# Optimization experiments

Measured on AMD Instinct MI355X. Metric: run time of the kernel, lower is better.

The kernel has to match this reference:

```python
import jax, jax.numpy as jnp
import numpy as np

FS = 512
SEQ_LEN = 16384
BATCH = 128
TAPS = 513  # common kernel length; per-band kernels zero-padded at the tail
N_BANDS = 20


def _design_kernels():
    """Windowed-sinc (fir1/firwin-style, hamming) bandpass kernels, tensorpac-like."""
    pha = [(f, f + 2.0) for f in np.arange(2.0, 22.0, 2.0)]    # 10 phase bands
    amp = [(f, f + 10.0) for f in np.arange(30.0, 130.0, 10.0)]  # 10 amp bands
    cycles = [3] * 10 + [6] * 10
    bands = pha + amp
    K = np.zeros((N_BANDS, TAPS), np.float32)
    for i, ((lo, hi), c) in enumerate(zip(bands, cycles)):
        order = min(int(c * FS / lo), TAPS - 1)  # fir_order ~ cycle * fs / low_hz
        taps = order + 1
        n = np.arange(taps) - (taps - 1) / 2.0
        f1, f2 = lo / FS, hi / FS
        h = 2.0 * f2 * np.sinc(2.0 * f2 * n) - 2.0 * f1 * np.sinc(2.0 * f1 * n)
        h *= np.hamming(taps)
        K[i, :taps] = h.astype(np.float32)
    return jnp.asarray(K)


def setup_inputs() -> dict:
    key = jax.random.key(0)
    x = jax.random.normal(key, (BATCH, 1, SEQ_LEN), dtype=jnp.float32)
    return {"x": x, "kernels": _design_kernels(), "padlen": TAPS - 1}


def _filtfilt_bands(x2d, kernels, P):
    """scipy.signal.filtfilt(b, 1.0, x, padlen=P) for all bands at once.
    x2d: (B, L); kernels: (nb, T) FIR taps. Odd-extension padding + lfilter_zi
    initial conditions (== constant extension of the first sample by T-1)."""
    B, L = x2d.shape
    nb, T = kernels.shape
    # odd extension: left_j = 2*x[0] - x[P-j], right_j = 2*x[-1] - x[-2-j]
    left = 2.0 * x2d[:, :1] - x2d[:, 1:P + 1][:, ::-1]
    right = 2.0 * x2d[:, -1:] - x2d[:, -P - 1:-1][:, ::-1]
    ext = jnp.concatenate([left, x2d, right], axis=1)  # (B, L + 2P)
    krev = kernels[:, ::-1][:, None, :]  # (nb, 1, T); correlation with b[::-1] == causal conv with b

    def causal_conv(sig, groups):
        # sig: (B, C, Ls); constant left-extension by T-1 (lfilter zi*x0 semantics)
        pad = jnp.repeat(sig[..., :1], T - 1, axis=-1)
        s = jnp.concatenate([pad, sig], axis=-1)
        return jax.lax.conv_general_dilated(
            s, krev, (1,), 'VALID',
            dimension_numbers=('NCW', 'OIW', 'NCW'),
            feature_group_count=groups)

    y = causal_conv(ext[:, None, :], 1)        # forward pass -> (B, nb, L+2P)
    y2 = causal_conv(y[:, :, ::-1], nb)        # backward pass (grouped, per-band)
    return y2[:, :, ::-1][:, :, P:P + L]       # un-reverse and trim padding


def reference(x, kernels, padlen):
    # x: (B, 1, L) -> (B, 1, n_bands, L)
    out = _filtfilt_bands(x[:, 0, :], kernels, padlen)
    return out[:, None, :, :]
```

## Files before the change

kernel.cpp:

```cpp
#include <hip/hip_runtime.h>

#define LSEQ   16384
#define NB     20
#define NBATCH 128
#define TAPS   513
#define CT     (2*TAPS - 1)
#define MAXSTEP 68

#define TT     2048
#define SPANE  3088
#define STRIDE 3096
#define EXTEND 16896
#define GMAX   17407

#define HDR_OFF  0
#define ATAB_OFF 1024

typedef short  v8s  __attribute__((ext_vector_type(8)));
typedef __bf16 v8bf __attribute__((ext_vector_type(8)));
typedef float  v16f __attribute__((ext_vector_type(16)));

__device__ __forceinline__ unsigned short f2bf(float f) {
    union { float f; unsigned u; } v; v.f = f;
    return (unsigned short)((v.u + 0x7fffu + ((v.u >> 16) & 1u)) >> 16);
}

__device__ __forceinline__ v16f vzero() {
    v16f z;
    #pragma unroll
    for (int i = 0; i < 16; ++i) z[i] = 0.f;
    return z;
}

__global__ __launch_bounds__(1024) void prep_kernel(
    const float* __restrict__ Kg, int2* __restrict__ hdr, short* __restrict__ atab)
{
    __shared__ float kk[TAPS];
    __shared__ float Cs[CT];
    __shared__ int smin, smax, sk0, sN;
    const int band = blockIdx.x;
    const int tid  = threadIdx.x;

    for (int i = tid; i < TAPS; i += 1024) kk[i] = Kg[band * TAPS + i];
    if (tid == 0) { smin = CT; smax = 0; }
    __syncthreads();

    int lmin = CT, lmax = 0;
    for (int d = tid; d < CT; d += 1024) {
        int al = d - 512; if (al < 0) al = -al;
        const int n = TAPS - al;
        float s0 = 0.f, s1 = 0.f, s2 = 0.f, s3 = 0.f;
        int i = 0;
        for (; i + 3 < n; i += 4) {
            s0 = fmaf(kk[i],     kk[i + al],     s0);
            s1 = fmaf(kk[i + 1], kk[i + 1 + al], s1);
            s2 = fmaf(kk[i + 2], kk[i + 2 + al], s2);
            s3 = fmaf(kk[i + 3], kk[i + 3 + al], s3);
        }
        for (; i < n; ++i) s0 = fmaf(kk[i], kk[i + al], s0);
        float s = (s0 + s1) + (s2 + s3);
        Cs[d] = s;
        if (s != 0.f) { if (d < lmin) lmin = d; if (d > lmax) lmax = d; }
    }
    atomicMin(&smin, lmin);
    atomicMax(&smax, lmax);
    __syncthreads();

    if (tid == 0) {
        int k0 = smin & ~15;
        int k1 = ((smax + 31) >> 4) << 4;
        int N  = (k1 - k0) / 16 + 1;
        int2 h; h.x = k0; h.y = N;
        hdr[band] = h;
        sk0 = k0; sN = N;
    }
    __syncthreads();

    const int k0 = sk0, N = sN;
    for (int idx = tid; idx < (N + 3) * 64; idx += 1024) {
        int s = idx >> 6, lane = idx & 63;
        int m = lane & 31, kh = lane >> 5;
        int base = k0 + 16 * s + 8 * kh - m;
        v8s r;
        #pragma unroll
        for (int j = 0; j < 8; ++j) {
            int ci = base + j;
            float v = (ci >= 0 && ci < CT) ? Cs[ci] : 0.f;
            r[j] = (short)f2bf(v);
        }
        *(v8s*)(atab + ((size_t)(band * MAXSTEP + s) * 64 + lane) * 8) = r;
    }
}

__global__ __launch_bounds__(256, 3) void filt_main(
    const float* __restrict__ x, const short* __restrict__ atab,
    const int2* __restrict__ hdr, float* __restrict__ out)
{
    __shared__ __align__(16) unsigned short extl[8 * STRIDE];
    const int tid = threadIdx.x;
    const int tile = blockIdx.x, grp = blockIdx.y, bg = blockIdx.z;
    const int T0 = tile * TT;

    const bool edge = (T0 < 512) || (T0 + SPANE > EXTEND);
    for (int b = 0; b < 8; ++b) {
        const float* xb = x + (size_t)(bg * 8 + b) * LSEQ;
        float x0 = 0.f, xN = 0.f;
        if (edge) { x0 = xb[0]; xN = xb[LSEQ - 1]; }
        for (int e4 = tid; e4 < SPANE / 4; e4 += 256) {
            const int e = 4 * e4;
            const int g0 = T0 + e;
            float v0, v1, v2, v3;
            if (g0 >= 512 && g0 + 4 <= EXTEND) {
                float4 xv = *(const float4*)(xb + (g0 - 512));
                v0 = xv.x; v1 = xv.y; v2 = xv.z; v3 = xv.w;
            } else {
                float vv[4];
                #pragma unroll
                for (int t = 0; t < 4; ++t) {
                    int g = g0 + t; if (g > GMAX) g = GMAX;
                    vv[t] = (g < 512)    ? 2.f * x0 - xb[512 - g]
                          : (g < EXTEND) ? xb[g - 512]
                          :                2.f * xN - xb[2 * LSEQ + 512 - 2 - g];
                }
                v0 = vv[0]; v1 = vv[1]; v2 = vv[2]; v3 = vv[3];
            }
            ushort4 q = make_ushort4(f2bf(v0), f2bf(v1), f2bf(v2), f2bf(v3));
            *(ushort4*)&extl[b * STRIDE + e] = q;
        }
    }
    __syncthreads();

    const int lane = tid & 63;
    const int w    = tid >> 6;
    const int n    = lane & 31, kh = lane >> 5;
    const int brow = n & 7,  tb = n >> 3;
    const unsigned short* bpb = extl + brow * STRIDE + 512 * w + 32 * tb + 8 * kh;

    const int g_start[6] = {0, 4, 8, 11, 15, 20};
    const int g_list[20] = {0,19,18,17, 1,16,15,14, 2,3,13, 4,5,6,12, 7,8,9,10,11};

    for (int bi = g_start[grp]; bi < g_start[grp + 1]; ++bi) {
        const int band = g_list[bi];
        const int2 hh = hdr[band];
        const int k0 = hh.x, N = hh.y;
        const unsigned short* bp = bpb + k0;
        const short* ap = atab + (size_t)(band * MAXSTEP) * 512 + lane * 8;

        v16f ac0 = vzero(), ac1 = vzero(), ac2 = vzero(), ac3 = vzero();
        v8bf A0 = __builtin_bit_cast(v8bf, *(const v8s*)ap);
        v8bf A1 = __builtin_bit_cast(v8bf, *(const v8s*)(ap + 512));
        v8bf A2 = __builtin_bit_cast(v8bf, *(const v8s*)(ap + 1024));
        v8bf B0 = *(const v8bf*)(bp);
        v8bf B1 = *(const v8bf*)(bp + 128);
        v8bf B2 = *(const v8bf*)(bp + 256);
        v8bf B3 = *(const v8bf*)(bp + 384);

        for (int s = 0; s < N; ++s) {
            v8bf An  = __builtin_bit_cast(v8bf, *(const v8s*)(ap + (size_t)(s + 3) * 512));
            const unsigned short* bn = bp + 16 * (s + 1);
            v8bf Bn0 = *(const v8bf*)(bn);
            v8bf Bn1 = *(const v8bf*)(bn + 128);
            v8bf Bn2 = *(const v8bf*)(bn + 256);
            v8bf Bn3 = *(const v8bf*)(bn + 384);
            ac0 = __builtin_amdgcn_mfma_f32_32x32x16_bf16(A0, B0, ac0, 0, 0, 0);
            ac1 = __builtin_amdgcn_mfma_f32_32x32x16_bf16(A0, B1, ac1, 0, 0, 0);
            ac2 = __builtin_amdgcn_mfma_f32_32x32x16_bf16(A0, B2, ac2, 0, 0, 0);
            ac3 = __builtin_amdgcn_mfma_f32_32x32x16_bf16(A0, B3, ac3, 0, 0, 0);
            A0 = A1; A1 = A2; A2 = An;
            B0 = Bn0; B1 = Bn1; B2 = Bn2; B3 = Bn3;
        }

        float* ob = out + ((size_t)(bg * 8 + brow) * NB + band) * LSEQ
                        + T0 + 512 * w + 32 * tb + 4 * kh;
        #pragma unroll
        for (int q = 0; q < 4; ++q) {
            *(float4*)(ob +       8 * q) = make_float4(ac0[4*q], ac0[4*q+1], ac0[4*q+2], ac0[4*q+3]);
            *(float4*)(ob + 128 + 8 * q) = make_float4(ac1[4*q], ac1[4*q+1], ac1[4*q+2], ac1[4*q+3]);
            *(float4*)(ob + 256 + 8 * q) = make_float4(ac2[4*q], ac2[4*q+1], ac2[4*q+2], ac2[4*q+3]);
            *(float4*)(ob + 384 + 8 * q) = make_float4(ac3[4*q], ac3[4*q+1], ac3[4*q+2], ac3[4*q+3]);
        }
    }
}

extern "C" void kernel_launch(void* const* d_in, const int* in_sizes, int n_in,
                              void* d_out, int out_size, void* d_ws, size_t ws_size,
                              hipStream_t stream) {
    const float* x  = (const float*)d_in[0];
    const float* Kg = (const float*)d_in[1];
    float* out = (float*)d_out;

    char* wsb = (char*)d_ws;
    int2*  hdr  = (int2*)(wsb + HDR_OFF);
    short* atab = (short*)(wsb + ATAB_OFF);

    prep_kernel<<<dim3(NB), dim3(1024), 0, stream>>>(Kg, hdr, atab);
    filt_main<<<dim3(LSEQ / TT, 5, NBATCH / 8), dim3(256), 0, stream>>>(x, atab, hdr, out);
}
```

Before: 229.0 us.

## Split kernel autocorrelation prep across more blocks and tune MFMA loop

The single 20-block prep kernel, which computed each band's kernel autocorrelation serially per lag, is split into two kernels. The first spreads lags over 9 blocks per band and splits each dot product four ways, reducing through shared memory. The second merges the per-block support bounds and builds the bf16 MFMA A-table. The main filter loop also gets unroll-by-2 and s_setprio around the MFMA group. This adds one extra launch and a workspace round-trip for the autocorrelation to shorten the prep critical path.

```diff
diff --git a/kernel.cpp b/kernel.cpp
--- a/kernel.cpp
+++ b/kernel.cpp
@@ -5,7 +5,7 @@
 #define NBATCH 128
 #define TAPS   513
 #define CT     (2*TAPS - 1)
-#define MAXSTEP 68
+#define MAXSTEP 72
 
 #define TT     2048
 #define SPANE  3088
@@ -14,7 +14,10 @@
 #define GMAX   17407
 
 #define HDR_OFF  0
-#define ATAB_OFF 1024
+#define MMX_OFF  256
+#define CS_OFF   4096
+#define CSTRIDE  1040
+#define ATAB_OFF 98304
 
 typedef short  v8s  __attribute__((ext_vector_type(8)));
 typedef __bf16 v8bf __attribute__((ext_vector_type(8)));
@@ -32,52 +35,74 @@
     return z;
 }
 
-__global__ __launch_bounds__(1024) void prep_kernel(
-    const float* __restrict__ Kg, int2* __restrict__ hdr, short* __restrict__ atab)
+__global__ __launch_bounds__(512) void autoc_kernel(
+    const float* __restrict__ Kg, float* __restrict__ Cs, int2* __restrict__ mmx)
 {
-    __shared__ float kk[TAPS];
-    __shared__ float Cs[CT];
-    __shared__ int smin, smax, sk0, sN;
-    const int band = blockIdx.x;
-    const int tid  = threadIdx.x;
-
-    for (int i = tid; i < TAPS; i += 1024) kk[i] = Kg[band * TAPS + i];
+    __shared__ __align__(16) float kk[TAPS];
+    __shared__ float ps[512];
+    __shared__ int smin, smax;
+    const int band = blockIdx.x, y = blockIdx.y;
+    const int tid = threadIdx.x;
+    const int rel = tid & 127, q = tid >> 7;
+    const int d = 128 * y + rel;
+
+    for (int i = tid; i < TAPS; i += 512) kk[i] = Kg[band * TAPS + i];
     if (tid == 0) { smin = CT; smax = 0; }
     __syncthreads();
 
-    int lmin = CT, lmax = 0;
-    for (int d = tid; d < CT; d += 1024) {
+    float s = 0.f;
+    if (d < CT) {
         int al = d - 512; if (al < 0) al = -al;
         const int n = TAPS - al;
+        const int nq = (((n + 3) >> 2) + 3) & ~3;
+        int i0 = q * nq, i1 = i0 + nq; if (i1 > n) i1 = n;
         float s0 = 0.f, s1 = 0.f, s2 = 0.f, s3 = 0.f;
-        int i = 0;
-        for (; i + 3 < n; i += 4) {
+        int i = i0;
+        for (; i + 3 < i1; i += 4) {
             s0 = fmaf(kk[i],     kk[i + al],     s0);
             s1 = fmaf(kk[i + 1], kk[i + 1 + al], s1);
             s2 = fmaf(kk[i + 2], kk[i + 2 + al], s2);
             s3 = fmaf(kk[i + 3], kk[i + 3 + al], s3);
         }
-        for (; i < n; ++i) s0 = fmaf(kk[i], kk[i + al], s0);
-        float s = (s0 + s1) + (s2 + s3);
-        Cs[d] = s;
-        if (s != 0.f) { if (d < lmin) lmin = d; if (d > lmax) lmax = d; }
-    }
-    atomicMin(&smin, lmin);
-    atomicMax(&smax, lmax);
-    __syncthreads();
-
+        for (; i < i1; ++i) s0 = fmaf(kk[i], kk[i + al], s0);
+        s = (s0 + s1) + (s2 + s3);
+    }
+    ps[tid] = s;
+    __syncthreads();
+    if (q == 0 && d < CT) {
+        float tot = (ps[rel] + ps[rel + 128]) + (ps[rel + 256] + ps[rel + 384]);
+        Cs[band * CSTRIDE + d] = tot;
+        if (tot != 0.f) { atomicMin(&smin, d); atomicMax(&smax, d); }
+    }
+    __syncthreads();
+    if (tid == 0) { int2 r; r.x = smin; r.y = smax; mmx[band * 9 + y] = r; }
+}
+
+__global__ __launch_bounds__(1024) void table_kernel(
+    const float* __restrict__ Cs, const int2* __restrict__ mmx,
+    int2* __restrict__ hdr, short* __restrict__ atab)
+{
+    __shared__ int sk0, sN;
+    const int band = blockIdx.x, tid = threadIdx.x;
     if (tid == 0) {
-        int k0 = smin & ~15;
-        int k1 = ((smax + 31) >> 4) << 4;
+        int mn = CT, mx = 0;
+        for (int j = 0; j < 9; ++j) {
+            int2 r = mmx[band * 9 + j];
+            if (r.x < mn) mn = r.x;
+            if (r.y > mx) mx = r.y;
+        }
+        int k0 = mn & ~15;
+        int k1 = ((mx + 31) >> 4) << 4;
         int N  = (k1 - k0) / 16 + 1;
         int2 h; h.x = k0; h.y = N;
         hdr[band] = h;
         sk0 = k0; sN = N;
     }
     __syncthreads();
-
     const int k0 = sk0, N = sN;
-    for (int idx = tid; idx < (N + 3) * 64; idx += 1024) {
+    int nf = N + 3; if (nf > MAXSTEP) nf = MAXSTEP;
+    const float* cb = Cs + band * CSTRIDE;
+    for (int idx = tid; idx < nf * 64; idx += 1024) {
         int s = idx >> 6, lane = idx & 63;
         int m = lane & 31, kh = lane >> 5;
         int base = k0 + 16 * s + 8 * kh - m;
@@ -85,7 +110,7 @@
         #pragma unroll
         for (int j = 0; j < 8; ++j) {
             int ci = base + j;
-            float v = (ci >= 0 && ci < CT) ? Cs[ci] : 0.f;
+            float v = (ci >= 0 && ci < CT) ? cb[ci] : 0.f;
             r[j] = (short)f2bf(v);
         }
         *(v8s*)(atab + ((size_t)(band * MAXSTEP + s) * 64 + lane) * 8) = r;
@@ -124,8 +149,8 @@
                 }
                 v0 = vv[0]; v1 = vv[1]; v2 = vv[2]; v3 = vv[3];
             }
-            ushort4 q = make_ushort4(f2bf(v0), f2bf(v1), f2bf(v2), f2bf(v3));
-            *(ushort4*)&extl[b * STRIDE + e] = q;
+            ushort4 qv = make_ushort4(f2bf(v0), f2bf(v1), f2bf(v2), f2bf(v3));
+            *(ushort4*)&extl[b * STRIDE + e] = qv;
         }
     }
     __syncthreads();
@@ -155,6 +180,7 @@
         v8bf B2 = *(const v8bf*)(bp + 256);
         v8bf B3 = *(const v8bf*)(bp + 384);
 
+        #pragma unroll 2
         for (int s = 0; s < N; ++s) {
             v8bf An  = __builtin_bit_cast(v8bf, *(const v8s*)(ap + (size_t)(s + 3) * 512));
             const unsigned short* bn = bp + 16 * (s + 1);
@@ -162,10 +188,12 @@
             v8bf Bn1 = *(const v8bf*)(bn + 128);
             v8bf Bn2 = *(const v8bf*)(bn + 256);
             v8bf Bn3 = *(const v8bf*)(bn + 384);
+            __builtin_amdgcn_s_setprio(1);
             ac0 = __builtin_amdgcn_mfma_f32_32x32x16_bf16(A0, B0, ac0, 0, 0, 0);
             ac1 = __builtin_amdgcn_mfma_f32_32x32x16_bf16(A0, B1, ac1, 0, 0, 0);
             ac2 = __builtin_amdgcn_mfma_f32_32x32x16_bf16(A0, B2, ac2, 0, 0, 0);
             ac3 = __builtin_amdgcn_mfma_f32_32x32x16_bf16(A0, B3, ac3, 0, 0, 0);
+            __builtin_amdgcn_s_setprio(0);
             A0 = A1; A1 = A2; A2 = An;
             B0 = Bn0; B1 = Bn1; B2 = Bn2; B3 = Bn3;
         }
@@ -191,8 +219,11 @@
 
     char* wsb = (char*)d_ws;
     int2*  hdr  = (int2*)(wsb + HDR_OFF);
+    int2*  mmx  = (int2*)(wsb + MMX_OFF);
+    float* Cs   = (float*)(wsb + CS_OFF);
     short* atab = (short*)(wsb + ATAB_OFF);
 
-    prep_kernel<<<dim3(NB), dim3(1024), 0, stream>>>(Kg, hdr, atab);
+    autoc_kernel<<<dim3(NB, 9), dim3(512), 0, stream>>>(Kg, Cs, mmx);
+    table_kernel<<<dim3(NB), dim3(1024), 0, stream>>>(Cs, mmx, hdr, atab);
     filt_main<<<dim3(LSEQ / TT, 5, NBATCH / 8), dim3(256), 0, stream>>>(x, atab, hdr, out);
 }
```

Result: faster. 223.1 us (-2.5%).
